# Performance work log

Hardware: AMD Instinct MI355X
Metric: run time of the kernel (lower is better)

The kernel has to match this reference:

```python
import jax, jax.numpy as jnp
import numpy as np

N = 50000      # nodes
E = 800000     # edges (avg degree 16)
IN, HID, OUT = 256, 128, 64
K, ALPHA = 4, 0.0  # APPNPConv(k=4, alpha=0.0)


def setup_inputs() -> dict:
    key = jax.random.key(0)
    ks = jax.random.split(key, 5)
    features = jax.random.normal(ks[0], (N, IN), jnp.float32)
    src = jax.random.randint(ks[1], (E,), 0, N, jnp.int32)
    dst = jax.random.randint(ks[2], (E,), 0, N, jnp.int32)
    W1 = jax.random.normal(ks[3], (IN, HID), jnp.float32) / np.float32(np.sqrt(IN))
    b1 = jnp.zeros((HID,), jnp.float32)
    W3 = jax.random.normal(ks[4], (HID, OUT), jnp.float32) / np.float32(np.sqrt(HID))
    b3 = jnp.zeros((OUT,), jnp.float32)
    return dict(features=features, src=src, dst=dst, W1=W1, b1=b1, W3=W3, b3=b3)


def _sym_norms(src, dst, n):
    # D_out^{-1/2} for source side, D_in^{-1/2} for destination side (DGL norm='both')
    ones = jnp.ones((src.shape[0],), jnp.float32)
    deg_out = jax.ops.segment_sum(ones, src, num_segments=n)
    deg_in = jax.ops.segment_sum(ones, dst, num_segments=n)
    return jnp.clip(deg_out, 1.0) ** -0.5, jnp.clip(deg_in, 1.0) ** -0.5


def _prop(x, src, dst, norm_src, norm_dst):
    # x: [N, D]. Symmetric-normalized SpMM: D_in^{-1/2} A D_out^{-1/2} x
    msg = (x * norm_src[:, None])[src]                       # [E, D] gather
    agg = jax.ops.segment_sum(msg, dst, num_segments=x.shape[0])  # [N, D] scatter-add
    return agg * norm_dst[:, None]


def reference(features, src, dst, W1, b1, W3, b3):
    ns, nd = _sym_norms(src, dst, N)
    # GraphConv 1 (weight-first since in_dim > hidden_dim; math identical either way)
    h = _prop(features @ W1, src, dst, ns, nd) + b1
    # dropout is identity in eval mode (training=False)
    # APPNPConv: k=4 power-iteration steps with teleport alpha=0.0
    h0 = h
    for _ in range(K):
        h = (1.0 - ALPHA) * _prop(h, src, dst, ns, nd) + ALPHA * h0
    # GraphConv 3
    out = _prop(h @ W3, src, dst, ns, nd) + b3
    return out
```

## Files before the change

### kernel.cpp

```cpp
#include <hip/hip_runtime.h>
#include <math.h>

#define N_NODES 50000
#define N_EDGES 800000
#define DIN 256
#define DHID 128
#define DOUT 64
#define CSTRIDE 64
#define ZROW N_NODES
#define HBLOCKS 128
#define HCHUNK (N_EDGES / HBLOCKS)
#define HWORDS (N_NODES / 4)
#define SLICE ((size_t)(N_NODES + 1) * 16)
#define NGROUPS (N_NODES / 4)
#define NPAIRS (NGROUPS / 2)
#define P2BLOCKS 196

#define SB_SENT 3125
#define SB_HS (SB_SENT + HBLOCKS)
#define SB_HD (SB_HS + HBLOCKS)
#define SB_TOT (SB_HD + 66)

__global__ void k_setup(const int* __restrict__ src, const int* __restrict__ dst,
                        unsigned int* __restrict__ pS, unsigned int* __restrict__ pD,
                        unsigned int* __restrict__ csr32,
                        const float* __restrict__ W1, const float* __restrict__ b1,
                        const float* __restrict__ W3,
                        float* __restrict__ W13, float* __restrict__ bb,
                        float* __restrict__ Y0, float* __restrict__ Y1) {
    __shared__ unsigned int h[HWORDS];
    int bx = blockIdx.x, t = threadIdx.x;
    if (bx < SB_SENT) {
        unsigned int v = (unsigned int)ZROW | ((unsigned int)ZROW << 16);
        uint2 o; o.x = v; o.y = v;
        ((uint2*)csr32)[bx * 256 + t] = o;
        return;
    }
    if (bx < SB_HD) {
        const int* idx = (bx < SB_HS) ? src : dst;
        unsigned int* outp = (bx < SB_HS) ? pS : pD;
        int hb = bx - ((bx < SB_HS) ? SB_SENT : SB_HS);
        for (int w = t; w < HWORDS; w += 256) h[w] = 0u;
        __syncthreads();
        int base = hb * HCHUNK;
        for (int i = t; i < HCHUNK; i += 256) {
            int s = idx[base + i];
            atomicAdd(&h[s >> 2], 1u << ((s & 3) << 3));
        }
        __syncthreads();
        outp += (size_t)hb * HWORDS;
        for (int w = t; w < HWORDS; w += 256) outp[w] = h[w];
        return;
    }
    int vb = bx - SB_HD;
    if (vb == 65) {
        if (t < 64) {
            int qq = t >> 4, c2 = t & 15;
            Y0[(size_t)qq * SLICE + ((size_t)ZROW << 4) + c2] = 0.f;
            Y1[(size_t)qq * SLICE + ((size_t)ZROW << 4) + c2] = 0.f;
        }
        return;
    }
    if (vb == 64) {
        if (t < DOUT) {
            float s = 0.f;
            for (int k = 0; k < DHID; ++k) s += b1[k] * W3[k * DOUT + t];
            bb[t] = s;
        }
        return;
    }
    int idx2 = vb * 256 + t;
    int i = idx2 >> 6, j = idx2 & 63;
    float s = 0.f;
    for (int k = 0; k < DHID; ++k) s += W1[i * DHID + k] * W3[k * DOUT + j];
    W13[idx2] = s;
}

__global__ void k_hpre(const unsigned int* __restrict__ pS,
                       const unsigned int* __restrict__ pD,
                       unsigned int* __restrict__ prefix,
                       int* __restrict__ deg_in,
                       float* __restrict__ ns, float* __restrict__ nd,
                       float* __restrict__ cc, int* __restrict__ dparts) {
    __shared__ unsigned int sdw[64][4];
    __shared__ unsigned int sow[64][4];
    __shared__ int lh[65];
    int t = threadIdx.x;
    if (t < 65) lh[t] = 0;
    int col = t >> 2, sub = t & 3;
    int wid = blockIdx.x * 64 + col;
    bool act = wid < HWORDS;
    unsigned int ps = 0, pd = 0;
    if (act) {
        int b0 = sub << 5;
#pragma unroll 4
        for (int b = b0; b < b0 + 32; ++b) {
            ps += pS[(size_t)b * HWORDS + wid];
            pd += pD[(size_t)b * HWORDS + wid];
        }
    }
    sdw[col][sub] = pd;
    sow[col][sub] = ps;
    __syncthreads();
    if (act) {
        unsigned int base = 0;
        for (int k = 0; k < sub; ++k) base += sdw[col][k];
        int b0 = sub << 5;
        unsigned int run = base;
        for (int b = b0; b < b0 + 32; ++b) {
            unsigned int w = pD[(size_t)b * HWORDS + wid];
            prefix[(size_t)b * HWORDS + wid] = run;
            run += w;
        }
        if (sub == 0) {
            unsigned int totd = sdw[col][0] + sdw[col][1] + sdw[col][2] + sdw[col][3];
            unsigned int toto = sow[col][0] + sow[col][1] + sow[col][2] + sow[col][3];
            unsigned int di[4] = {totd & 0xffu, (totd >> 8) & 0xffu,
                                  (totd >> 16) & 0xffu, totd >> 24};
            unsigned int dov[4] = {toto & 0xffu, (toto >> 8) & 0xffu,
                                   (toto >> 16) & 0xffu, toto >> 24};
            int4 dd; dd.x = (int)di[0]; dd.y = (int)di[1]; dd.z = (int)di[2]; dd.w = (int)di[3];
            *(int4*)(deg_in + (wid << 2)) = dd;
            float4 vns, vnd, vcc;
            float* pns = &vns.x; float* pnd = &vnd.x; float* pcc = &vcc.x;
#pragma unroll
            for (int q = 0; q < 4; ++q) {
                int bin = (int)di[q]; if (bin > 64) bin = 64;
                atomicAdd(&lh[bin], 1);
                unsigned int a = dov[q] < 1u ? 1u : dov[q];
                unsigned int b = di[q] < 1u ? 1u : di[q];
                float fa = 1.0f / sqrtf((float)a);
                float fb = 1.0f / sqrtf((float)b);
                pns[q] = fa; pnd[q] = fb; pcc[q] = fa * fb;
            }
            *(float4*)(ns + (wid << 2)) = vns;
            *(float4*)(nd + (wid << 2)) = vnd;
            *(float4*)(cc + (wid << 2)) = vcc;
        }
    }
    __syncthreads();
    if (t < 65) dparts[blockIdx.x * 65 + t] = lh[t];
}

__global__ void k_dscatter(const int* __restrict__ deg_in, const int* __restrict__ dparts,
                           const float* __restrict__ cc, const float* __restrict__ ns,
                           const float* __restrict__ nd,
                           int* __restrict__ perm, int* __restrict__ inv,
                           int* __restrict__ degP, float* __restrict__ ccP,
                           float* __restrict__ nsP, float* __restrict__ ndP) {
    __shared__ int colsum[65], pre[65], off[65];
    int t = threadIdx.x;
    if (t < 65) {
        int tot = 0, pr = 0;
        int mybx = (int)blockIdx.x;
        for (int b = 0; b < P2BLOCKS; ++b) {
            int v = dparts[b * 65 + t];
            tot += v;
            if (b < mybx) pr += v;
        }
        colsum[t] = tot; pre[t] = pr;
    }
    __syncthreads();
    if (t == 0) {
        int run = 0;
        for (int k = 64; k >= 0; --k) { int c = colsum[k]; colsum[k] = run; run += c; }
    }
    __syncthreads();
    if (t < 65) off[t] = colsum[t] + pre[t];
    __syncthreads();
    int wid = blockIdx.x * 64 + t;
    if (t < 64 && wid < HWORDS) {
        int4 d4 = *(const int4*)(deg_in + (wid << 2));
        int dd[4] = {d4.x, d4.y, d4.z, d4.w};
#pragma unroll
        for (int k = 0; k < 4; ++k) {
            int node = (wid << 2) + k;
            int bin = dd[k] > 64 ? 64 : dd[k];
            int slot = atomicAdd(&off[bin], 1);
            perm[slot] = node; inv[node] = slot;
            degP[slot] = dd[k];
            ccP[slot] = cc[node]; nsP[slot] = ns[node]; ndP[slot] = nd[node];
        }
    }
}

__global__ void k_fill(const int* __restrict__ src, const int* __restrict__ dst,
                       const unsigned int* __restrict__ prefix,
                       const int* __restrict__ inv,
                       unsigned short* __restrict__ csr) {
    __shared__ unsigned int h[HWORDS];
    int t = threadIdx.x;
    const unsigned int* prow = prefix + (size_t)blockIdx.x * HWORDS;
    for (int w = t; w < HWORDS; w += 256) h[w] = prow[w];
    __syncthreads();
    int base = blockIdx.x * HCHUNK;
    for (int i = t; i < HCHUNK; i += 256) {
        int s = src[base + i], d = dst[base + i];
        int sh = (d & 3) << 3;
        unsigned int old = atomicAdd(&h[d >> 2], 1u << sh);
        int slot = (int)((old >> sh) & 0xffu);
        csr[((size_t)inv[d] << 6) + slot] = (unsigned short)inv[s];
    }
}

__global__ void k_gemm(const float* __restrict__ X, const float* __restrict__ W13,
                       const float* __restrict__ ns, const int* __restrict__ inv,
                       float* __restrict__ Y) {
    __shared__ float As[16][68];
    __shared__ float Bs[16][64];
    int tid = threadIdx.x;
    int tx = tid & 15, ty = tid >> 4;
    int row0 = blockIdx.x * 64;
    float acc[4][4];
#pragma unroll
    for (int i = 0; i < 4; ++i)
#pragma unroll
        for (int j = 0; j < 4; ++j) acc[i][j] = 0.f;

    int lr = tid >> 2;
    int lk = (tid & 3) << 2;
    int arow = row0 + lr;
    if (arow > N_NODES - 1) arow = N_NODES - 1;

    for (int k0 = 0; k0 < DIN; k0 += 16) {
        float4 a = *(const float4*)(X + (size_t)arow * DIN + k0 + lk);
        As[lk + 0][lr] = a.x; As[lk + 1][lr] = a.y;
        As[lk + 2][lr] = a.z; As[lk + 3][lr] = a.w;
        float4 b = *(const float4*)(W13 + (size_t)(k0 + (tid >> 4)) * DOUT + ((tid & 15) << 2));
        *(float4*)&Bs[tid >> 4][(tid & 15) << 2] = b;
        __syncthreads();
#pragma unroll
        for (int k = 0; k < 16; ++k) {
            float4 av = *(const float4*)&As[k][ty << 2];
            float4 bv = *(const float4*)&Bs[k][tx << 2];
            float ar[4] = {av.x, av.y, av.z, av.w};
            float br[4] = {bv.x, bv.y, bv.z, bv.w};
#pragma unroll
            for (int i = 0; i < 4; ++i)
#pragma unroll
                for (int j = 0; j < 4; ++j) acc[i][j] += ar[i] * br[j];
        }
        __syncthreads();
    }
    int qq = tx >> 2;
    int co = (tx & 3) << 2;
#pragma unroll
    for (int i = 0; i < 4; ++i) {
        int row = row0 + (ty << 2) + i;
        if (row < N_NODES) {
            float nsr = ns[row];
            int prow = inv[row];
            float4 o;
            o.x = acc[i][0] * nsr; o.y = acc[i][1] * nsr;
            o.z = acc[i][2] * nsr; o.w = acc[i][3] * nsr;
            *(float4*)(Y + (size_t)qq * SLICE + ((size_t)prow << 4) + co) = o;
        }
    }
}


template <int MODE>
__launch_bounds__(256, 8)
__global__ void k_spmm(const float* __restrict__ xs, float* __restrict__ ys,
                       const unsigned short* __restrict__ csr,
                       const int* __restrict__ degP,
                       const float* __restrict__ ccP, const float* __restrict__ nsP,
                       const float* __restrict__ ndP,
                       const float* __restrict__ bb, const float* __restrict__ b3,
                       const int* __restrict__ perm) {
    __shared__ unsigned short rows[4][512];
    int wid  = threadIdx.x >> 6;
    int lane = threadIdx.x & 63;
    int q    = (blockIdx.x & 7) >> 1;
    int half = blockIdx.x & 1;
    int p    = (blockIdx.x >> 3) * 8 + wid * 2 + half;
    if (p >= NPAIRS) return;
    int node0 = p << 3;

    int nn = lane >> 4, sl = lane & 15;
    const uint2* crowA = (const uint2*)(csr + ((size_t)(node0 + nn) << 6)) + sl;
    const uint2* crowB = (const uint2*)(csr + ((size_t)(node0 + 4 + nn) << 6)) + sl;
    uint2 rva = *crowA;
    uint2 rvb = *crowB;
    unsigned short* bpA = &rows[wid][(sl << 4) + nn];
    unsigned short* bpB = bpA + 256;
    bpA[0]  = (unsigned short)(rva.x & 0xffffu);
    bpA[4]  = (unsigned short)(rva.x >> 16);
    bpA[8]  = (unsigned short)(rva.y & 0xffffu);
    bpA[12] = (unsigned short)(rva.y >> 16);
    bpB[0]  = (unsigned short)(rvb.x & 0xffffu);
    bpB[4]  = (unsigned short)(rvb.x >> 16);
    bpB[8]  = (unsigned short)(rvb.y & 0xffffu);
    bpB[12] = (unsigned short)(rvb.y >> 16);

    int n0u = __builtin_amdgcn_readfirstlane(node0);
    int m = (degP[n0u] + 7) & ~7;

    int n = lane >> 4, e = (lane >> 2) & 3, c4 = lane & 3;
    const unsigned short* rdA = &rows[wid][(e << 2) + n];
    const unsigned short* rdB = rdA + 256;
    const float* xq = xs + (size_t)q * SLICE + (c4 << 2);

    float aAx = 0.f, aAy = 0.f, aAz = 0.f, aAw = 0.f;
    float aBx = 0.f, aBy = 0.f, aBz = 0.f, aBw = 0.f;
#define LDA(T) const float4 vA##T = *(const float4*)(xq + ((size_t)rdA[16 * (T)] << 4))
#define LDB(T) const float4 vB##T = *(const float4*)(xq + ((size_t)rdB[16 * (T)] << 4))
#define ACA(T) aAx += vA##T.x; aAy += vA##T.y; aAz += vA##T.z; aAw += vA##T.w
#define ACB(T) aBx += vB##T.x; aBy += vB##T.y; aBz += vB##T.z; aBw += vB##T.w
    if (m <= 8) {
        LDA(0); LDA(1); LDB(0); LDB(1);
        ACA(0); ACA(1); ACB(0); ACB(1);
    } else if (m <= 16) {
        LDA(0); LDA(1); LDA(2); LDA(3); LDB(0); LDB(1); LDB(2); LDB(3);
        ACA(0); ACA(1); ACA(2); ACA(3); ACB(0); ACB(1); ACB(2); ACB(3);
    } else if (m <= 24) {
        LDA(0); LDA(1); LDA(2); LDA(3); LDA(4); LDA(5);
        LDB(0); LDB(1);
        ACA(0); ACA(1); ACA(2); ACA(3);
        LDB(2); LDB(3); LDB(4); LDB(5);
        ACA(4); ACA(5);
        ACB(0); ACB(1); ACB(2); ACB(3); ACB(4); ACB(5);
    } else if (m <= 32) {
        LDA(0); LDA(1); LDA(2); LDA(3); LDB(0); LDB(1); LDB(2); LDB(3);
        ACA(0); ACA(1); ACA(2); ACA(3); ACB(0); ACB(1); ACB(2); ACB(3);
        LDA(4); LDA(5); LDA(6); LDA(7); LDB(4); LDB(5); LDB(6); LDB(7);
        ACA(4); ACA(5); ACA(6); ACA(7); ACB(4); ACB(5); ACB(6); ACB(7);
    } else {
        for (int j2 = 0; j2 < m; j2 += 8) {
            int o = j2 << 2;
            const float4 a0 = *(const float4*)(xq + ((size_t)rdA[o] << 4));
            const float4 a1 = *(const float4*)(xq + ((size_t)rdA[o + 16] << 4));
            const float4 b0 = *(const float4*)(xq + ((size_t)rdB[o] << 4));
            const float4 b1 = *(const float4*)(xq + ((size_t)rdB[o + 16] << 4));
            aAx += a0.x; aAy += a0.y; aAz += a0.z; aAw += a0.w;
            aAx += a1.x; aAy += a1.y; aAz += a1.z; aAw += a1.w;
            aBx += b0.x; aBy += b0.y; aBz += b0.z; aBw += b0.w;
            aBx += b1.x; aBy += b1.y; aBz += b1.z; aBw += b1.w;
        }
    }
#undef LDA
#undef LDB
#undef ACA
#undef ACB
    aAx += __shfl_xor(aAx, 4);  aAy += __shfl_xor(aAy, 4);
    aAz += __shfl_xor(aAz, 4);  aAw += __shfl_xor(aAw, 4);
    aBx += __shfl_xor(aBx, 4);  aBy += __shfl_xor(aBy, 4);
    aBz += __shfl_xor(aBz, 4);  aBw += __shfl_xor(aBw, 4);
    aAx += __shfl_xor(aAx, 8);  aAy += __shfl_xor(aAy, 8);
    aAz += __shfl_xor(aAz, 8);  aAw += __shfl_xor(aAw, 8);
    aBx += __shfl_xor(aBx, 8);  aBy += __shfl_xor(aBy, 8);
    aBz += __shfl_xor(aBz, 8);  aBw += __shfl_xor(aBw, 8);

    int nodeA = node0 + n;
    int nodeB = node0 + 4 + n;
    int colq  = (q << 4) + (c4 << 2);
    float4 rA, rB;
    if (MODE == 0) {
        float4 bv = *(const float4*)(bb + colq);
        float cvA = ccP[nodeA], nvA = nsP[nodeA];
        rA.x = cvA * aAx + nvA * bv.x; rA.y = cvA * aAy + nvA * bv.y;
        rA.z = cvA * aAz + nvA * bv.z; rA.w = cvA * aAw + nvA * bv.w;
        float cvB = ccP[nodeB], nvB = nsP[nodeB];
        rB.x = cvB * aBx + nvB * bv.x; rB.y = cvB * aBy + nvB * bv.y;
        rB.z = cvB * aBz + nvB * bv.z; rB.w = cvB * aBw + nvB * bv.w;
    } else if (MODE == 1) {
        float cvA = ccP[nodeA];
        rA.x = cvA * aAx; rA.y = cvA * aAy; rA.z = cvA * aAz; rA.w = cvA * aAw;
        float cvB = ccP[nodeB];
        rB.x = cvB * aBx; rB.y = cvB * aBy; rB.z = cvB * aBz; rB.w = cvB * aBw;
    } else {
        float4 bv = *(const float4*)(b3 + colq);
        float dvA = ndP[nodeA];
        rA.x = dvA * aAx + bv.x; rA.y = dvA * aAy + bv.y;
        rA.z = dvA * aAz + bv.z; rA.w = dvA * aAw + bv.w;
        float dvB = ndP[nodeB];
        rB.x = dvB * aBx + bv.x; rB.y = dvB * aBy + bv.y;
        rB.z = dvB * aBz + bv.z; rB.w = dvB * aBw + bv.w;
    }
    if (e == 0) {
        if (MODE == 2) {
            int orowA = perm[nodeA];
            int orowB = perm[nodeB];
            *(float4*)(ys + ((size_t)orowA << 6) + colq) = rA;
            *(float4*)(ys + ((size_t)orowB << 6) + colq) = rB;
        } else {
            *(float4*)(ys + (size_t)q * SLICE + ((size_t)nodeA << 4) + (c4 << 2)) = rA;
            *(float4*)(ys + (size_t)q * SLICE + ((size_t)nodeB << 4) + (c4 << 2)) = rB;
        }
    }
}


extern "C" void kernel_launch(void* const* d_in, const int* in_sizes, int n_in,
                              void* d_out, int out_size, void* d_ws, size_t ws_size,
                              hipStream_t stream) {
    const float* X   = (const float*)d_in[0];
    const int*   src = (const int*)d_in[1];
    const int*   dst = (const int*)d_in[2];
    const float* W1  = (const float*)d_in[3];
    const float* b1  = (const float*)d_in[4];
    const float* W3  = (const float*)d_in[5];
    const float* b3  = (const float*)d_in[6];
    float* out = (float*)d_out;

    char* ws = (char*)d_ws;
    size_t off = 0;
    auto alloc = [&](size_t bytes) -> void* {
        void* p = ws + off;
        off = (off + bytes + 255) & ~(size_t)255;
        return p;
    };
    unsigned int*   pS     = (unsigned int*)alloc((size_t)HBLOCKS * HWORDS * 4);
    unsigned int*   pD     = (unsigned int*)alloc((size_t)HBLOCKS * HWORDS * 4);
    unsigned int*   pref   = (unsigned int*)alloc((size_t)HBLOCKS * HWORDS * 4);
    float*          Y0     = (float*)alloc(SLICE * 4 * 4);
    float*          Y1     = (float*)alloc(SLICE * 4 * 4);
    unsigned short* csr    = (unsigned short*)alloc((size_t)N_NODES * CSTRIDE * 2);
    int*            deg_in = (int*)alloc((size_t)N_NODES * 4);
    float*          ns     = (float*)alloc((size_t)N_NODES * 4);
    float*          nd     = (float*)alloc((size_t)N_NODES * 4);
    float*          cc     = (float*)alloc((size_t)N_NODES * 4);
    int*            perm   = (int*)alloc((size_t)N_NODES * 4);
    int*            inv    = (int*)alloc((size_t)N_NODES * 4);
    int*            degP   = (int*)alloc((size_t)N_NODES * 4);
    float*          ccP    = (float*)alloc((size_t)N_NODES * 4);
    float*          nsP    = (float*)alloc((size_t)N_NODES * 4);
    float*          ndP    = (float*)alloc((size_t)N_NODES * 4);
    int*            dparts = (int*)alloc((size_t)P2BLOCKS * 65 * 4);
    float*          W13    = (float*)alloc((size_t)DIN * DOUT * 4);
    float*          bb     = (float*)alloc(DOUT * 4);

    const int sblk = 782 * 8;

    k_setup<<<SB_TOT, 256, 0, stream>>>(src, dst, pS, pD, (unsigned int*)csr,
                                        W1, b1, W3, W13, bb, Y0, Y1);
    k_hpre<<<P2BLOCKS, 256, 0, stream>>>(pS, pD, pref, deg_in, ns, nd, cc, dparts);
    k_dscatter<<<P2BLOCKS, 128, 0, stream>>>(deg_in, dparts, cc, ns, nd,
                                             perm, inv, degP, ccP, nsP, ndP);
    k_fill<<<HBLOCKS, 256, 0, stream>>>(src, dst, pref, inv, csr);

    k_gemm<<<(N_NODES + 63) / 64, 256, 0, stream>>>(X, W13, ns, inv, Y0);

    k_spmm<0><<<sblk, 256, 0, stream>>>(Y0, Y1, csr, degP, ccP, nsP, ndP, bb, b3, perm);
    k_spmm<1><<<sblk, 256, 0, stream>>>(Y1, Y0, csr, degP, ccP, nsP, ndP, bb, b3, perm);
    k_spmm<1><<<sblk, 256, 0, stream>>>(Y0, Y1, csr, degP, ccP, nsP, ndP, bb, b3, perm);
    k_spmm<1><<<sblk, 256, 0, stream>>>(Y1, Y0, csr, degP, ccP, nsP, ndP, bb, b3, perm);
    k_spmm<1><<<sblk, 256, 0, stream>>>(Y0, Y1, csr, degP, ccP, nsP, ndP, bb, b3, perm);
    k_spmm<2><<<sblk, 256, 0, stream>>>(Y1, out, csr, degP, ccP, nsP, ndP, bb, b3, perm);
}
```

Before: 309.4 us.

## Widen feature slices from 16 to 32 columns in SpMM layout

Changes the intermediate feature layout from four 16-column slices to two 32-column slices, so each gathered neighbor row is a full 128-byte line. Each wave now handles more node pairs per slice, with 8 lanes per node covering 32 columns and half as many lanes splitting edges. The CSR row is loaded as uint4, the number of SpMM blocks is halved, and one shuffle-reduction stage is dropped. The aim is fewer partial-line gather transactions and less duplicated CSR/index work per edge, at the cost of more sequential loads per lane.

```diff
diff --git a/kernel.cpp b/kernel.cpp
--- a/kernel.cpp
+++ b/kernel.cpp
@@ -11,7 +11,7 @@
 #define HBLOCKS 128
 #define HCHUNK (N_EDGES / HBLOCKS)
 #define HWORDS (N_NODES / 4)
-#define SLICE ((size_t)(N_NODES + 1) * 16)
+#define SLICE2 ((size_t)(N_NODES + 1) * 32)
 #define NGROUPS (N_NODES / 4)
 #define NPAIRS (NGROUPS / 2)
 #define P2BLOCKS 196
@@ -55,9 +55,9 @@
     int vb = bx - SB_HD;
     if (vb == 65) {
         if (t < 64) {
-            int qq = t >> 4, c2 = t & 15;
-            Y0[(size_t)qq * SLICE + ((size_t)ZROW << 4) + c2] = 0.f;
-            Y1[(size_t)qq * SLICE + ((size_t)ZROW << 4) + c2] = 0.f;
+            int q2 = t >> 5, c2 = t & 31;
+            Y0[(size_t)q2 * SLICE2 + ((size_t)ZROW << 5) + c2] = 0.f;
+            Y1[(size_t)q2 * SLICE2 + ((size_t)ZROW << 5) + c2] = 0.f;
         }
         return;
     }
@@ -253,7 +253,8 @@
             float4 o;
             o.x = acc[i][0] * nsr; o.y = acc[i][1] * nsr;
             o.z = acc[i][2] * nsr; o.w = acc[i][3] * nsr;
-            *(float4*)(Y + (size_t)qq * SLICE + ((size_t)prow << 4) + co) = o;
+            *(float4*)(Y + (size_t)(qq >> 1) * SLICE2 + ((size_t)prow << 5)
+                       + ((qq & 1) << 4) + co) = o;
         }
     }
 }
@@ -271,81 +272,88 @@
     __shared__ unsigned short rows[4][512];
     int wid  = threadIdx.x >> 6;
     int lane = threadIdx.x & 63;
-    int q    = (blockIdx.x & 7) >> 1;
-    int half = blockIdx.x & 1;
-    int p    = (blockIdx.x >> 3) * 8 + wid * 2 + half;
+    int bx   = (int)blockIdx.x;
+    int q2   = (bx >> 2) & 1;
+    int p    = (bx >> 3) * 16 + wid * 4 + (bx & 3);
     if (p >= NPAIRS) return;
     int node0 = p << 3;
 
-    int nn = lane >> 4, sl = lane & 15;
-    const uint2* crowA = (const uint2*)(csr + ((size_t)(node0 + nn) << 6)) + sl;
-    const uint2* crowB = (const uint2*)(csr + ((size_t)(node0 + 4 + nn) << 6)) + sl;
-    uint2 rva = *crowA;
-    uint2 rvb = *crowB;
-    unsigned short* bpA = &rows[wid][(sl << 4) + nn];
-    unsigned short* bpB = bpA + 256;
-    bpA[0]  = (unsigned short)(rva.x & 0xffffu);
-    bpA[4]  = (unsigned short)(rva.x >> 16);
-    bpA[8]  = (unsigned short)(rva.y & 0xffffu);
-    bpA[12] = (unsigned short)(rva.y >> 16);
-    bpB[0]  = (unsigned short)(rvb.x & 0xffffu);
-    bpB[4]  = (unsigned short)(rvb.x >> 16);
-    bpB[8]  = (unsigned short)(rvb.y & 0xffffu);
-    bpB[12] = (unsigned short)(rvb.y >> 16);
+    int nn = lane >> 3, sl = lane & 7;
+    const uint4* crow = (const uint4*)(csr + ((size_t)(node0 + nn) << 6)) + sl;
+    uint4 rv = *crow;
+    unsigned short* bp = &rows[wid][((nn >> 2) << 8) + (sl << 5) + (nn & 3)];
+    bp[0]  = (unsigned short)(rv.x & 0xffffu);
+    bp[4]  = (unsigned short)(rv.x >> 16);
+    bp[8]  = (unsigned short)(rv.y & 0xffffu);
+    bp[12] = (unsigned short)(rv.y >> 16);
+    bp[16] = (unsigned short)(rv.z & 0xffffu);
+    bp[20] = (unsigned short)(rv.z >> 16);
+    bp[24] = (unsigned short)(rv.w & 0xffffu);
+    bp[28] = (unsigned short)(rv.w >> 16);
 
     int n0u = __builtin_amdgcn_readfirstlane(node0);
     int m = (degP[n0u] + 7) & ~7;
 
-    int n = lane >> 4, e = (lane >> 2) & 3, c4 = lane & 3;
+    int n = lane >> 4, e = (lane >> 3) & 1, c8 = lane & 7;
     const unsigned short* rdA = &rows[wid][(e << 2) + n];
     const unsigned short* rdB = rdA + 256;
-    const float* xq = xs + (size_t)q * SLICE + (c4 << 2);
+    const float* xq = xs + (size_t)q2 * SLICE2 + (c8 << 2);
 
     float aAx = 0.f, aAy = 0.f, aAz = 0.f, aAw = 0.f;
     float aBx = 0.f, aBy = 0.f, aBz = 0.f, aBw = 0.f;
-#define LDA(T) const float4 vA##T = *(const float4*)(xq + ((size_t)rdA[16 * (T)] << 4))
-#define LDB(T) const float4 vB##T = *(const float4*)(xq + ((size_t)rdB[16 * (T)] << 4))
+#define LDA(T) const float4 vA##T = *(const float4*)(xq + ((size_t)rdA[8 * (T)] << 5))
+#define LDB(T) const float4 vB##T = *(const float4*)(xq + ((size_t)rdB[8 * (T)] << 5))
 #define ACA(T) aAx += vA##T.x; aAy += vA##T.y; aAz += vA##T.z; aAw += vA##T.w
 #define ACB(T) aBx += vB##T.x; aBy += vB##T.y; aBz += vB##T.z; aBw += vB##T.w
     if (m <= 8) {
-        LDA(0); LDA(1); LDB(0); LDB(1);
-        ACA(0); ACA(1); ACB(0); ACB(1);
+        LDA(0); LDA(1); LDA(2); LDA(3); LDB(0); LDB(1); LDB(2); LDB(3);
+        ACA(0); ACA(1); ACA(2); ACA(3); ACB(0); ACB(1); ACB(2); ACB(3);
     } else if (m <= 16) {
         LDA(0); LDA(1); LDA(2); LDA(3); LDB(0); LDB(1); LDB(2); LDB(3);
-        ACA(0); ACA(1); ACA(2); ACA(3); ACB(0); ACB(1); ACB(2); ACB(3);
+        LDA(4); LDA(5); LDA(6); LDA(7); ACA(0); ACA(1); ACA(2); ACA(3);
+        LDB(4); LDB(5); LDB(6); LDB(7); ACB(0); ACB(1); ACB(2); ACB(3);
+        ACA(4); ACA(5); ACA(6); ACA(7); ACB(4); ACB(5); ACB(6); ACB(7);
     } else if (m <= 24) {
-        LDA(0); LDA(1); LDA(2); LDA(3); LDA(4); LDA(5);
-        LDB(0); LDB(1);
-        ACA(0); ACA(1); ACA(2); ACA(3);
-        LDB(2); LDB(3); LDB(4); LDB(5);
-        ACA(4); ACA(5);
-        ACB(0); ACB(1); ACB(2); ACB(3); ACB(4); ACB(5);
+        LDA(0); LDA(1); LDA(2); LDA(3); LDB(0); LDB(1); LDB(2); LDB(3);
+        LDA(4); LDA(5); LDA(6); LDA(7); ACA(0); ACA(1); ACA(2); ACA(3);
+        LDB(4); LDB(5); LDB(6); LDB(7); ACB(0); ACB(1); ACB(2); ACB(3);
+        LDA(8); LDA(9); LDA(10); LDA(11); ACA(4); ACA(5); ACA(6); ACA(7);
+        LDB(8); LDB(9); LDB(10); LDB(11); ACB(4); ACB(5); ACB(6); ACB(7);
+        ACA(8); ACA(9); ACA(10); ACA(11); ACB(8); ACB(9); ACB(10); ACB(11);
     } else if (m <= 32) {
         LDA(0); LDA(1); LDA(2); LDA(3); LDB(0); LDB(1); LDB(2); LDB(3);
-        ACA(0); ACA(1); ACA(2); ACA(3); ACB(0); ACB(1); ACB(2); ACB(3);
-        LDA(4); LDA(5); LDA(6); LDA(7); LDB(4); LDB(5); LDB(6); LDB(7);
-        ACA(4); ACA(5); ACA(6); ACA(7); ACB(4); ACB(5); ACB(6); ACB(7);
+        LDA(4); LDA(5); LDA(6); LDA(7); ACA(0); ACA(1); ACA(2); ACA(3);
+        LDB(4); LDB(5); LDB(6); LDB(7); ACB(0); ACB(1); ACB(2); ACB(3);
+        LDA(8); LDA(9); LDA(10); LDA(11); ACA(4); ACA(5); ACA(6); ACA(7);
+        LDB(8); LDB(9); LDB(10); LDB(11); ACB(4); ACB(5); ACB(6); ACB(7);
+        LDA(12); LDA(13); LDA(14); LDA(15); ACA(8); ACA(9); ACA(10); ACA(11);
+        LDB(12); LDB(13); LDB(14); LDB(15); ACB(8); ACB(9); ACB(10); ACB(11);
+        ACA(12); ACA(13); ACA(14); ACA(15); ACB(12); ACB(13); ACB(14); ACB(15);
     } else {
         for (int j2 = 0; j2 < m; j2 += 8) {
             int o = j2 << 2;
-            const float4 a0 = *(const float4*)(xq + ((size_t)rdA[o] << 4));
-            const float4 a1 = *(const float4*)(xq + ((size_t)rdA[o + 16] << 4));
-            const float4 b0 = *(const float4*)(xq + ((size_t)rdB[o] << 4));
-            const float4 b1 = *(const float4*)(xq + ((size_t)rdB[o + 16] << 4));
+            const float4 a0 = *(const float4*)(xq + ((size_t)rdA[o] << 5));
+            const float4 a1 = *(const float4*)(xq + ((size_t)rdA[o + 8] << 5));
+            const float4 a2 = *(const float4*)(xq + ((size_t)rdA[o + 16] << 5));
+            const float4 a3 = *(const float4*)(xq + ((size_t)rdA[o + 24] << 5));
+            const float4 b0 = *(const float4*)(xq + ((size_t)rdB[o] << 5));
+            const float4 b1 = *(const float4*)(xq + ((size_t)rdB[o + 8] << 5));
+            const float4 b2 = *(const float4*)(xq + ((size_t)rdB[o + 16] << 5));
+            const float4 b3v = *(const float4*)(xq + ((size_t)rdB[o + 24] << 5));
             aAx += a0.x; aAy += a0.y; aAz += a0.z; aAw += a0.w;
             aAx += a1.x; aAy += a1.y; aAz += a1.z; aAw += a1.w;
+            aAx += a2.x; aAy += a2.y; aAz += a2.z; aAw += a2.w;
+            aAx += a3.x; aAy += a3.y; aAz += a3.z; aAw += a3.w;
             aBx += b0.x; aBy += b0.y; aBz += b0.z; aBw += b0.w;
             aBx += b1.x; aBy += b1.y; aBz += b1.z; aBw += b1.w;
+            aBx += b2.x; aBy += b2.y; aBz += b2.z; aBw += b2.w;
+            aBx += b3v.x; aBy += b3v.y; aBz += b3v.z; aBw += b3v.w;
         }
     }
 #undef LDA
 #undef LDB
 #undef ACA
 #undef ACB
-    aAx += __shfl_xor(aAx, 4);  aAy += __shfl_xor(aAy, 4);
-    aAz += __shfl_xor(aAz, 4);  aAw += __shfl_xor(aAw, 4);
-    aBx += __shfl_xor(aBx, 4);  aBy += __shfl_xor(aBy, 4);
-    aBz += __shfl_xor(aBz, 4);  aBw += __shfl_xor(aBw, 4);
     aAx += __shfl_xor(aAx, 8);  aAy += __shfl_xor(aAy, 8);
     aAz += __shfl_xor(aAz, 8);  aAw += __shfl_xor(aAw, 8);
     aBx += __shfl_xor(aBx, 8);  aBy += __shfl_xor(aBy, 8);
@@ -353,7 +361,7 @@
 
     int nodeA = node0 + n;
     int nodeB = node0 + 4 + n;
-    int colq  = (q << 4) + (c4 << 2);
+    int colq  = (q2 << 5) + (c8 << 2);
     float4 rA, rB;
     if (MODE == 0) {
         float4 bv = *(const float4*)(bb + colq);
@@ -384,8 +392,8 @@
             *(float4*)(ys + ((size_t)orowA << 6) + colq) = rA;
             *(float4*)(ys + ((size_t)orowB << 6) + colq) = rB;
         } else {
-            *(float4*)(ys + (size_t)q * SLICE + ((size_t)nodeA << 4) + (c4 << 2)) = rA;
-            *(float4*)(ys + (size_t)q * SLICE + ((size_t)nodeB << 4) + (c4 << 2)) = rB;
+            *(float4*)(ys + (size_t)q2 * SLICE2 + ((size_t)nodeA << 5) + (c8 << 2)) = rA;
+            *(float4*)(ys + (size_t)q2 * SLICE2 + ((size_t)nodeB << 5) + (c8 << 2)) = rB;
         }
     }
 }
@@ -413,8 +421,8 @@
     unsigned int*   pS     = (unsigned int*)alloc((size_t)HBLOCKS * HWORDS * 4);
     unsigned int*   pD     = (unsigned int*)alloc((size_t)HBLOCKS * HWORDS * 4);
     unsigned int*   pref   = (unsigned int*)alloc((size_t)HBLOCKS * HWORDS * 4);
-    float*          Y0     = (float*)alloc(SLICE * 4 * 4);
-    float*          Y1     = (float*)alloc(SLICE * 4 * 4);
+    float*          Y0     = (float*)alloc(SLICE2 * 2 * 4);
+    float*          Y1     = (float*)alloc(SLICE2 * 2 * 4);
     unsigned short* csr    = (unsigned short*)alloc((size_t)N_NODES * CSTRIDE * 2);
     int*            deg_in = (int*)alloc((size_t)N_NODES * 4);
     float*          ns     = (float*)alloc((size_t)N_NODES * 4);
@@ -430,7 +438,7 @@
     float*          W13    = (float*)alloc((size_t)DIN * DOUT * 4);
     float*          bb     = (float*)alloc(DOUT * 4);
 
-    const int sblk = 782 * 8;
+    const int sblk = 391 * 8;
 
     k_setup<<<SB_TOT, 256, 0, stream>>>(src, dst, pS, pD, (unsigned int*)csr,
                                         W1, b1, W3, W13, bb, Y0, Y1);
```

New measurement: 303.7 us. Within noise of the previous version (-1.8%).
